# Kernel tuning notes

Measured on AMD Instinct MI355X. Metric: run time of the kernel, lower is better.

Reference implementation:

```python
import jax, jax.numpy as jnp
import numpy as np

N_NODES = 50000
N_EDGES = 800000
D = 64
BN_EPS = 1e-5


def setup_inputs() -> dict:
    key = jax.random.key(0)
    ks = jax.random.split(key, 16)
    x = jax.random.normal(ks[0], (N_NODES, D), dtype=jnp.float32)
    edge_index = jax.random.randint(ks[1], (2, N_EDGES), 0, N_NODES, dtype=jnp.int64)
    s = 1.0 / np.sqrt(D)
    def lin(k):
        kw, kb = jax.random.split(k)
        W = jax.random.uniform(kw, (D, D), jnp.float32, -s, s)
        b = jax.random.uniform(kb, (D,), jnp.float32, -s, s)
        return W, b
    W1_0, b1_0 = lin(ks[2])
    W2_0, b2_0 = lin(ks[3])
    W1_1, b1_1 = lin(ks[4])
    W2_1, b2_1 = lin(ks[5])
    return {
        "x": x, "edge_index": edge_index,
        "W1_0": W1_0, "b1_0": b1_0, "g_0": jnp.ones((D,), jnp.float32), "beta_0": jnp.zeros((D,), jnp.float32), "W2_0": W2_0, "b2_0": b2_0,
        "W1_1": W1_1, "b1_1": b1_1, "g_1": jnp.ones((D,), jnp.float32), "beta_1": jnp.zeros((D,), jnp.float32), "W2_1": W2_1, "b2_1": b2_1,
    }


def _gin_layer(x, src, dst, W1, b1, g, beta, W2, b2):
    # GINConv with eps=0: h_i = MLP( x_i + sum_{j->i} x_j )
    agg = jax.ops.segment_sum(x[src], dst, num_segments=N_NODES)  # [N, D]
    h = agg + x
    h = h @ W1 + b1
    # BatchNorm1d (training-mode batch statistics, biased variance)
    mean = jnp.mean(h, axis=0)
    var = jnp.var(h, axis=0)
    h = (h - mean) * jax.lax.rsqrt(var + BN_EPS) * g + beta
    h = jax.nn.relu(h)
    h = jax.nn.relu(h @ W2 + b2)
    return h


def reference(x, edge_index, W1_0, b1_0, g_0, beta_0, W2_0, b2_0,
              W1_1, b1_1, g_1, beta_1, W2_1, b2_1):
    src = edge_index[0]  # message source j
    dst = edge_index[1]  # aggregation target i
    h1 = _gin_layer(x, src, dst, W1_0, b1_0, g_0, beta_0, W2_0, b2_0)
    h2 = _gin_layer(h1, src, dst, W1_1, b1_1, g_1, beta_1, W2_1, b2_1)
    return (h1, h2)
```

## Files before the change

### kernel.cpp

```cpp
#include <hip/hip_runtime.h>
#include <hip/hip_bf16.h>

#define N_NODES 50000
#define N_EDGES 800000
#define DD 64
#define RPB 64
#define GBLOCKS ((N_NODES + RPB - 1) / RPB)
#define SCAN_BLOCKS ((N_NODES + 255) / 256)
#define BN_EPS 1e-5f


__device__ __forceinline__ float bf2f(unsigned short b) {
    return __uint_as_float(((unsigned)b) << 16);
}
__device__ __forceinline__ float loadF(const void* p, int i, int isf) {
    return isf ? ((const float*)p)[i] : bf2f(((const unsigned short*)p)[i]);
}
template<bool ISF>
__device__ __forceinline__ float4 ld4(const void* p, int i) {
    if (ISF) return *reinterpret_cast<const float4*>((const float*)p + i);
    ushort4 u = *reinterpret_cast<const ushort4*>((const unsigned short*)p + i);
    return make_float4(bf2f(u.x), bf2f(u.y), bf2f(u.z), bf2f(u.w));
}
__device__ __forceinline__ void acc8(float4& a, float4& b, uint4 u) {
    a.x += __uint_as_float(u.x << 16);
    a.y += __uint_as_float(u.x & 0xFFFF0000u);
    a.z += __uint_as_float(u.y << 16);
    a.w += __uint_as_float(u.y & 0xFFFF0000u);
    b.x += __uint_as_float(u.z << 16);
    b.y += __uint_as_float(u.z & 0xFFFF0000u);
    b.z += __uint_as_float(u.w << 16);
    b.w += __uint_as_float(u.w & 0xFFFF0000u);
}

__global__ void init_kernel(const void* __restrict__ x, const int* __restrict__ ei,
                            int* __restrict__ flags, int* __restrict__ cnt,
                            float* __restrict__ sums) {
    int i = blockIdx.x * 256 + threadIdx.x;
    if (i < N_NODES) cnt[i] = 0;
    if (i < 128) sums[i] = 0.0f;
    if (blockIdx.x == 0) {
        __shared__ int cntF, cntI;
        int t = threadIdx.x;
        if (t == 0) { cntF = 0; cntI = 0; }
        __syncthreads();
        unsigned short w = ((const unsigned short*)x)[2 * t];
        int e = (w >> 7) & 0xFF;
        if (e >= 0x70 && e <= 0x8F) atomicAdd(&cntF, 1);
        if (t < 128 && ei[2 * t + 1] == 0) atomicAdd(&cntI, 1);
        __syncthreads();
        if (t == 0) {
            flags[0] = (cntF < 128) ? 1 : 0;
            flags[1] = (cntI > 64) ? 1 : 0;
        }
    }
}

__global__ void cast_kernel(const void* __restrict__ x, unsigned short* __restrict__ xb,
                            const int* __restrict__ flags) {
    int isf = flags[0];
    int i = (blockIdx.x * 256 + threadIdx.x) * 8;
    if (i >= N_NODES * DD) return;
    if (isf) {
        float4 a = *reinterpret_cast<const float4*>((const float*)x + i);
        float4 b = *reinterpret_cast<const float4*>((const float*)x + i + 4);
        ushort4 o0, o1;
        o0.x = __bfloat16_as_ushort(__float2bfloat16(a.x));
        o0.y = __bfloat16_as_ushort(__float2bfloat16(a.y));
        o0.z = __bfloat16_as_ushort(__float2bfloat16(a.z));
        o0.w = __bfloat16_as_ushort(__float2bfloat16(a.w));
        o1.x = __bfloat16_as_ushort(__float2bfloat16(b.x));
        o1.y = __bfloat16_as_ushort(__float2bfloat16(b.y));
        o1.z = __bfloat16_as_ushort(__float2bfloat16(b.z));
        o1.w = __bfloat16_as_ushort(__float2bfloat16(b.w));
        *reinterpret_cast<ushort4*>(xb + i) = o0;
        *reinterpret_cast<ushort4*>(xb + i + 4) = o1;
    } else {
        *reinterpret_cast<uint4*>(xb + i) =
            *reinterpret_cast<const uint4*>((const unsigned short*)x + i);
    }
}

__global__ void hist_kernel(const int* __restrict__ ei, int* __restrict__ cnt,
                            const int* __restrict__ flags) {
    int i64 = flags[1];
    int e = blockIdx.x * 256 + threadIdx.x;
    int d = i64 ? ei[2 * N_EDGES + 2 * e] : ei[N_EDGES + e];
    atomicAdd(cnt + d, 1);
}

__global__ __launch_bounds__(256) void scanA_kernel(const int* __restrict__ cnt,
                                                    int* __restrict__ off,
                                                    int* __restrict__ bsum) {
    __shared__ int tmp[256];
    int t = threadIdx.x;
    int i = blockIdx.x * 256 + t;
    int v = (i < N_NODES) ? cnt[i] : 0;
    tmp[t] = v;
    __syncthreads();
    #pragma unroll
    for (int d = 1; d < 256; d <<= 1) {
        int u = (t >= d) ? tmp[t - d] : 0;
        __syncthreads();
        tmp[t] += u;
        __syncthreads();
    }
    if (i < N_NODES) off[i] = tmp[t] - v;
    if (t == 255) bsum[blockIdx.x] = tmp[255];
}

__global__ __launch_bounds__(256) void scanB_kernel(int* __restrict__ bsum,
                                                    int* __restrict__ off) {
    __shared__ int tmp[256];
    int t = threadIdx.x;
    int v = (t < SCAN_BLOCKS) ? bsum[t] : 0;
    tmp[t] = v;
    __syncthreads();
    #pragma unroll
    for (int d = 1; d < 256; d <<= 1) {
        int u = (t >= d) ? tmp[t - d] : 0;
        __syncthreads();
        tmp[t] += u;
        __syncthreads();
    }
    if (t < SCAN_BLOCKS) bsum[t] = tmp[t] - v;
    if (t == 255) off[N_NODES] = tmp[255];
}

__global__ __launch_bounds__(256) void scanC_kernel(const int* __restrict__ bsum,
                                                    int* __restrict__ off,
                                                    int* __restrict__ cur) {
    int i = blockIdx.x * 256 + threadIdx.x;
    if (i < N_NODES) {
        int o = off[i] + bsum[blockIdx.x];
        off[i] = o;
        cur[i] = o;
    }
}

__global__ void fill_kernel(const int* __restrict__ ei, int* __restrict__ cur,
                            int* __restrict__ srt, const int* __restrict__ flags) {
    int i64 = flags[1];
    int e = blockIdx.x * 256 + threadIdx.x;
    int s, d;
    if (i64) { s = ei[2 * e]; d = ei[2 * N_EDGES + 2 * e]; }
    else     { s = ei[e];     d = ei[N_EDGES + e]; }
    int pos = atomicAdd(cur + d, 1);
    srt[pos] = s;
}

__global__ __launch_bounds__(512) void gather_gemm_stats_kernel(
    const unsigned short* __restrict__ xb, const void* __restrict__ self_src, int force_f32,
    const int* __restrict__ off, const int* __restrict__ srt,
    const void* __restrict__ W, const void* __restrict__ bias,
    float* __restrict__ out_, float* __restrict__ sums, const int* __restrict__ flags)
{
    __shared__ float sIn[RPB][DD];
    __shared__ float r1[8][DD], r2[8][DD];
    int tid = threadIdx.x;
    int lane = tid & 63, w = tid >> 6;
    int rs = lane >> 3, ch = lane & 7;
    int row0 = blockIdx.x * RPB;
    int isf = force_f32 ? 1 : flags[0];

    int lr = w * 8 + rs;
    int r = row0 + lr;
    float4 a  = make_float4(0.f, 0.f, 0.f, 0.f);
    float4 b  = make_float4(0.f, 0.f, 0.f, 0.f);
    float4 a2 = make_float4(0.f, 0.f, 0.f, 0.f);
    float4 b2 = make_float4(0.f, 0.f, 0.f, 0.f);
    if (r < N_NODES) {
        a = isf ? ld4<true>(self_src, r * DD + 8 * ch)
                : ld4<false>(self_src, r * DD + 8 * ch);
        b = isf ? ld4<true>(self_src, r * DD + 8 * ch + 4)
                : ld4<false>(self_src, r * DD + 8 * ch + 4);
        int k0 = off[r], k1 = off[r + 1];
        int k = k0;
        for (; k + 4 <= k1; k += 4) {
            int n0 = srt[k], n1 = srt[k + 1], n2 = srt[k + 2], n3 = srt[k + 3];
            uint4 u0 = *reinterpret_cast<const uint4*>(xb + n0 * DD + 8 * ch);
            uint4 u1 = *reinterpret_cast<const uint4*>(xb + n1 * DD + 8 * ch);
            uint4 u2 = *reinterpret_cast<const uint4*>(xb + n2 * DD + 8 * ch);
            uint4 u3 = *reinterpret_cast<const uint4*>(xb + n3 * DD + 8 * ch);
            acc8(a, b, u0);
            acc8(a2, b2, u1);
            acc8(a, b, u2);
            acc8(a2, b2, u3);
        }
        for (; k < k1; ++k) {
            int n0 = srt[k];
            acc8(a, b, *reinterpret_cast<const uint4*>(xb + n0 * DD + 8 * ch));
        }
        a.x += a2.x; a.y += a2.y; a.z += a2.z; a.w += a2.w;
        b.x += b2.x; b.y += b2.y; b.z += b2.z; b.w += b2.w;
    }
    *reinterpret_cast<float4*>(&sIn[lr][8 * ch]) = a;
    *reinterpret_cast<float4*>(&sIn[lr][8 * ch + 4]) = b;
    __syncthreads();

    float wcol[DD];
    #pragma unroll
    for (int k = 0; k < DD; ++k) wcol[k] = loadF(W, k * DD + lane, isf);
    float bv = loadF(bias, lane, isf);

    float s1 = 0.f, s2 = 0.f;
    #pragma unroll 4
    for (int j = 0; j < 8; ++j) {
        int jr = w * 8 + j;
        float c0 = 0.f, c1 = 0.f, c2 = 0.f, c3 = 0.f;
        #pragma unroll
        for (int k = 0; k < DD; k += 4) {
            float4 aa = *reinterpret_cast<const float4*>(&sIn[jr][k]);
            c0 += aa.x * wcol[k];
            c1 += aa.y * wcol[k + 1];
            c2 += aa.z * wcol[k + 2];
            c3 += aa.w * wcol[k + 3];
        }
        float acc = bv + ((c0 + c1) + (c2 + c3));
        int rr = row0 + jr;
        if (rr < N_NODES) {
            out_[rr * DD + lane] = acc;
            s1 += acc;
            s2 += acc * acc;
        }
    }
    r1[w][lane] = s1; r2[w][lane] = s2;
    __syncthreads();
    if (w == 0) {
        float t1 = 0.f, t2 = 0.f;
        #pragma unroll
        for (int q = 0; q < 8; ++q) { t1 += r1[q][lane]; t2 += r2[q][lane]; }
        atomicAdd(&sums[lane], t1);
        atomicAdd(&sums[64 + lane], t2);
    }
}

__global__ void bn_params_kernel(float* __restrict__ sums,
                                 const void* __restrict__ gma, const void* __restrict__ beta,
                                 float* __restrict__ scsh, const int* __restrict__ flags) {
    int isf = flags[0];
    int c = threadIdx.x;
    float S1 = sums[c];
    float S2 = sums[64 + c];
    float mean = S1 * (1.0f / N_NODES);
    float var  = S2 * (1.0f / N_NODES) - mean * mean;
    float scale = rsqrtf(var + BN_EPS) * loadF(gma, c, isf);
    scsh[c] = scale;
    scsh[DD + c] = loadF(beta, c, isf) - mean * scale;
    sums[c] = 0.0f;
    sums[64 + c] = 0.0f;
}

__global__ __launch_bounds__(256) void mlp2_kernel(
    const float* __restrict__ in_, const float* __restrict__ scsh,
    const void* __restrict__ W, const void* __restrict__ bias,
    float* __restrict__ oF, unsigned short* obf, const int* __restrict__ flags)
{
    __shared__ float sIn[RPB][DD];
    int isf = flags[0];
    int tid = threadIdx.x;
    int c = tid & 63, g = tid >> 6;
    int row0 = blockIdx.x * RPB;

    #pragma unroll
    for (int j = 0; j < 4; ++j) {
        int lr = (tid >> 4) + 16 * j;
        int cc = (tid & 15) << 2;
        int r = row0 + lr;
        float4 v = make_float4(0.f, 0.f, 0.f, 0.f);
        if (r < N_NODES) {
            v = *reinterpret_cast<const float4*>(in_ + r * DD + cc);
            float4 sc = *reinterpret_cast<const float4*>(scsh + cc);
            float4 sh = *reinterpret_cast<const float4*>(scsh + DD + cc);
            v.x = fmaxf(v.x * sc.x + sh.x, 0.f);
            v.y = fmaxf(v.y * sc.y + sh.y, 0.f);
            v.z = fmaxf(v.z * sc.z + sh.z, 0.f);
            v.w = fmaxf(v.w * sc.w + sh.w, 0.f);
        }
        *reinterpret_cast<float4*>(&sIn[lr][cc]) = v;
    }
    __syncthreads();

    float wcol[DD];
    #pragma unroll
    for (int k = 0; k < DD; ++k) wcol[k] = loadF(W, k * DD + c, isf);
    float bv = loadF(bias, c, isf);

    #pragma unroll 4
    for (int j = 0; j < 16; ++j) {
        int lr = g * 16 + j;
        float a0 = 0.f, a1 = 0.f, a2 = 0.f, a3 = 0.f;
        #pragma unroll
        for (int k = 0; k < DD; k += 4) {
            float4 a = *reinterpret_cast<const float4*>(&sIn[lr][k]);
            a0 += a.x * wcol[k];
            a1 += a.y * wcol[k + 1];
            a2 += a.z * wcol[k + 2];
            a3 += a.w * wcol[k + 3];
        }
        float acc = fmaxf(bv + ((a0 + a1) + (a2 + a3)), 0.f);
        int r = row0 + lr;
        if (r < N_NODES) {
            oF[r * DD + c] = acc;
            if (obf) obf[r * DD + c] = __bfloat16_as_ushort(__float2bfloat16(acc));
        }
    }
}

extern "C" void kernel_launch(void* const* d_in, const int* in_sizes, int n_in,
                              void* d_out, int out_size, void* d_ws, size_t ws_size,
                              hipStream_t stream)
{
    (void)in_sizes; (void)n_in; (void)out_size; (void)ws_size;
    const void* x  = d_in[0];
    const int* ei  = (const int*)d_in[1];
    const void* W1_0 = d_in[2];  const void* b1_0 = d_in[3];
    const void* g_0  = d_in[4];  const void* be_0 = d_in[5];
    const void* W2_0 = d_in[6];  const void* b2_0 = d_in[7];
    const void* W1_1 = d_in[8];  const void* b1_1 = d_in[9];
    const void* g_1  = d_in[10]; const void* be_1 = d_in[11];
    const void* W2_1 = d_in[12]; const void* b2_1 = d_in[13];

    float* wsf  = (float*)d_ws;
    float* sums = wsf;
    float* scsh = wsf + 128;
    int*  flags = (int*)(wsf + 256);
    int*  cnt   = (int*)(wsf + 512);
    int*  off   = cnt + 50048;
    int*  cur   = off + 50064;
    int*  bsum  = cur + 50048;
    int*  srt   = bsum + 256;
    unsigned short* xb = (unsigned short*)(srt + 800000);
    float* O1   = (float*)d_out;
    float* O2   = O1 + (size_t)N_NODES * DD;

    dim3 blk(256);

    init_kernel<<<SCAN_BLOCKS, blk, 0, stream>>>(x, ei, flags, cnt, sums);
    cast_kernel<<<(N_NODES * DD / 8 + 255) / 256, blk, 0, stream>>>(x, xb, flags);
    hist_kernel<<<N_EDGES / 256, blk, 0, stream>>>(ei, cnt, flags);
    scanA_kernel<<<SCAN_BLOCKS, blk, 0, stream>>>(cnt, off, bsum);
    scanB_kernel<<<1, blk, 0, stream>>>(bsum, off);
    scanC_kernel<<<SCAN_BLOCKS, blk, 0, stream>>>(bsum, off, cur);
    fill_kernel<<<N_EDGES / 256, blk, 0, stream>>>(ei, cur, srt, flags);

    gather_gemm_stats_kernel<<<GBLOCKS, 512, 0, stream>>>(xb, x, 0, off, srt, W1_0, b1_0,
                                                          O2, sums, flags);
    bn_params_kernel<<<1, 64, 0, stream>>>(sums, g_0, be_0, scsh, flags);
    mlp2_kernel<<<GBLOCKS, blk, 0, stream>>>(O2, scsh, W2_0, b2_0, O1, xb, flags);

    gather_gemm_stats_kernel<<<GBLOCKS, 512, 0, stream>>>(xb, O1, 1, off, srt, W1_1, b1_1,
                                                          O2, sums, flags);
    bn_params_kernel<<<1, 64, 0, stream>>>(sums, g_1, be_1, scsh, flags);
    mlp2_kernel<<<GBLOCKS, blk, 0, stream>>>(O2, scsh, W2_1, b2_1, O2, nullptr, flags);
}
```

Measured before the change: 320.9 us.

## Fuse init/cast and BN-param kernels, halve gather rows, use 16-bit neighbor indices

Merges the init and cast kernels into one launch, and folds the BN scale/shift computation into each mlp2 block so the single-thread bn_params launches go away. Separate stat buffers per layer replace the zero-reset. The gather kernel now handles 32 rows per block with two lanes per row splitting the edge list, combined by a shuffle, to raise parallelism. Sorted source indices are stored as 16-bit values to cut index traffic. This relies on node ids fitting in 16 bits, but there are 50000 nodes, which is below 65536. Every mlp2 block also recomputes the BN params redundantly.

```diff
diff --git a/kernel.cpp b/kernel.cpp
--- a/kernel.cpp
+++ b/kernel.cpp
@@ -4,9 +4,11 @@
 #define N_NODES 50000
 #define N_EDGES 800000
 #define DD 64
-#define RPB 64
+#define RPB 32
 #define GBLOCKS ((N_NODES + RPB - 1) / RPB)
+#define MBLOCKS ((N_NODES + 63) / 64)
 #define SCAN_BLOCKS ((N_NODES + 255) / 256)
+#define CAST_BLOCKS ((N_NODES * DD / 8 + 255) / 256)
 #define BN_EPS 1e-5f
 
 
@@ -33,51 +35,50 @@
     b.w += __uint_as_float(u.w & 0xFFFF0000u);
 }
 
-__global__ void init_kernel(const void* __restrict__ x, const int* __restrict__ ei,
-                            int* __restrict__ flags, int* __restrict__ cnt,
-                            float* __restrict__ sums) {
-    int i = blockIdx.x * 256 + threadIdx.x;
-    if (i < N_NODES) cnt[i] = 0;
-    if (i < 128) sums[i] = 0.0f;
-    if (blockIdx.x == 0) {
-        __shared__ int cntF, cntI;
-        int t = threadIdx.x;
-        if (t == 0) { cntF = 0; cntI = 0; }
-        __syncthreads();
-        unsigned short w = ((const unsigned short*)x)[2 * t];
-        int e = (w >> 7) & 0xFF;
-        if (e >= 0x70 && e <= 0x8F) atomicAdd(&cntF, 1);
-        if (t < 128 && ei[2 * t + 1] == 0) atomicAdd(&cntI, 1);
-        __syncthreads();
-        if (t == 0) {
-            flags[0] = (cntF < 128) ? 1 : 0;
-            flags[1] = (cntI > 64) ? 1 : 0;
-        }
-    }
-}
-
-__global__ void cast_kernel(const void* __restrict__ x, unsigned short* __restrict__ xb,
-                            const int* __restrict__ flags) {
-    int isf = flags[0];
-    int i = (blockIdx.x * 256 + threadIdx.x) * 8;
-    if (i >= N_NODES * DD) return;
-    if (isf) {
-        float4 a = *reinterpret_cast<const float4*>((const float*)x + i);
-        float4 b = *reinterpret_cast<const float4*>((const float*)x + i + 4);
-        ushort4 o0, o1;
-        o0.x = __bfloat16_as_ushort(__float2bfloat16(a.x));
-        o0.y = __bfloat16_as_ushort(__float2bfloat16(a.y));
-        o0.z = __bfloat16_as_ushort(__float2bfloat16(a.z));
-        o0.w = __bfloat16_as_ushort(__float2bfloat16(a.w));
-        o1.x = __bfloat16_as_ushort(__float2bfloat16(b.x));
-        o1.y = __bfloat16_as_ushort(__float2bfloat16(b.y));
-        o1.z = __bfloat16_as_ushort(__float2bfloat16(b.z));
-        o1.w = __bfloat16_as_ushort(__float2bfloat16(b.w));
-        *reinterpret_cast<ushort4*>(xb + i) = o0;
-        *reinterpret_cast<ushort4*>(xb + i + 4) = o1;
-    } else {
-        *reinterpret_cast<uint4*>(xb + i) =
-            *reinterpret_cast<const uint4*>((const unsigned short*)x + i);
+__global__ __launch_bounds__(256) void initcast_kernel(
+    const void* __restrict__ x, const int* __restrict__ ei,
+    int* __restrict__ flags, int* __restrict__ cnt,
+    float* __restrict__ sums, unsigned short* __restrict__ xb)
+{
+    __shared__ int cntF, cntI;
+    int t = threadIdx.x;
+    if (t == 0) { cntF = 0; cntI = 0; }
+    __syncthreads();
+    unsigned short wd = ((const unsigned short*)x)[2 * t];
+    int e = (wd >> 7) & 0xFF;
+    if (e >= 0x70 && e <= 0x8F) atomicAdd(&cntF, 1);
+    if (t < 128 && ei[2 * t + 1] == 0) atomicAdd(&cntI, 1);
+    __syncthreads();
+    int isf = (cntF < 128) ? 1 : 0;
+
+    int gid = blockIdx.x * 256 + t;
+    if (gid < N_NODES) cnt[gid] = 0;
+    if (gid < 256) sums[gid] = 0.0f;
+    if (blockIdx.x == 0 && t == 0) {
+        flags[0] = isf;
+        flags[1] = (cntI > 64) ? 1 : 0;
+    }
+
+    int i = gid * 8;
+    if (i < N_NODES * DD) {
+        if (isf) {
+            float4 a = *reinterpret_cast<const float4*>((const float*)x + i);
+            float4 b = *reinterpret_cast<const float4*>((const float*)x + i + 4);
+            ushort4 o0, o1;
+            o0.x = __bfloat16_as_ushort(__float2bfloat16(a.x));
+            o0.y = __bfloat16_as_ushort(__float2bfloat16(a.y));
+            o0.z = __bfloat16_as_ushort(__float2bfloat16(a.z));
+            o0.w = __bfloat16_as_ushort(__float2bfloat16(a.w));
+            o1.x = __bfloat16_as_ushort(__float2bfloat16(b.x));
+            o1.y = __bfloat16_as_ushort(__float2bfloat16(b.y));
+            o1.z = __bfloat16_as_ushort(__float2bfloat16(b.z));
+            o1.w = __bfloat16_as_ushort(__float2bfloat16(b.w));
+            *reinterpret_cast<ushort4*>(xb + i) = o0;
+            *reinterpret_cast<ushort4*>(xb + i + 4) = o1;
+        } else {
+            *reinterpret_cast<uint4*>(xb + i) =
+                *reinterpret_cast<const uint4*>((const unsigned short*)x + i);
+        }
     }
 }
 
@@ -139,19 +140,19 @@
 }
 
 __global__ void fill_kernel(const int* __restrict__ ei, int* __restrict__ cur,
-                            int* __restrict__ srt, const int* __restrict__ flags) {
+                            unsigned short* __restrict__ srt, const int* __restrict__ flags) {
     int i64 = flags[1];
     int e = blockIdx.x * 256 + threadIdx.x;
     int s, d;
     if (i64) { s = ei[2 * e]; d = ei[2 * N_EDGES + 2 * e]; }
     else     { s = ei[e];     d = ei[N_EDGES + e]; }
     int pos = atomicAdd(cur + d, 1);
-    srt[pos] = s;
+    srt[pos] = (unsigned short)s;
 }
 
 __global__ __launch_bounds__(512) void gather_gemm_stats_kernel(
     const unsigned short* __restrict__ xb, const void* __restrict__ self_src, int force_f32,
-    const int* __restrict__ off, const int* __restrict__ srt,
+    const int* __restrict__ off, const unsigned short* __restrict__ srt,
     const void* __restrict__ W, const void* __restrict__ bias,
     float* __restrict__ out_, float* __restrict__ sums, const int* __restrict__ flags)
 {
@@ -159,43 +160,55 @@
     __shared__ float r1[8][DD], r2[8][DD];
     int tid = threadIdx.x;
     int lane = tid & 63, w = tid >> 6;
-    int rs = lane >> 3, ch = lane & 7;
+    int rs = lane >> 4;
+    int ns = (lane >> 3) & 1;
+    int ch = lane & 7;
     int row0 = blockIdx.x * RPB;
     int isf = force_f32 ? 1 : flags[0];
 
-    int lr = w * 8 + rs;
+    int lr = w * 4 + rs;
     int r = row0 + lr;
     float4 a  = make_float4(0.f, 0.f, 0.f, 0.f);
     float4 b  = make_float4(0.f, 0.f, 0.f, 0.f);
     float4 a2 = make_float4(0.f, 0.f, 0.f, 0.f);
     float4 b2 = make_float4(0.f, 0.f, 0.f, 0.f);
     if (r < N_NODES) {
-        a = isf ? ld4<true>(self_src, r * DD + 8 * ch)
-                : ld4<false>(self_src, r * DD + 8 * ch);
-        b = isf ? ld4<true>(self_src, r * DD + 8 * ch + 4)
-                : ld4<false>(self_src, r * DD + 8 * ch + 4);
+        if (ns == 0) {
+            a = isf ? ld4<true>(self_src, r * DD + 8 * ch)
+                    : ld4<false>(self_src, r * DD + 8 * ch);
+            b = isf ? ld4<true>(self_src, r * DD + 8 * ch + 4)
+                    : ld4<false>(self_src, r * DD + 8 * ch + 4);
+        }
         int k0 = off[r], k1 = off[r + 1];
-        int k = k0;
-        for (; k + 4 <= k1; k += 4) {
-            int n0 = srt[k], n1 = srt[k + 1], n2 = srt[k + 2], n3 = srt[k + 3];
+        int mid = k0 + ((k1 - k0 + 1) >> 1);
+        int k  = ns ? mid : k0;
+        int ke = ns ? k1 : mid;
+        for (; k + 2 <= ke; k += 2) {
+            int n0 = srt[k], n1 = srt[k + 1];
             uint4 u0 = *reinterpret_cast<const uint4*>(xb + n0 * DD + 8 * ch);
             uint4 u1 = *reinterpret_cast<const uint4*>(xb + n1 * DD + 8 * ch);
-            uint4 u2 = *reinterpret_cast<const uint4*>(xb + n2 * DD + 8 * ch);
-            uint4 u3 = *reinterpret_cast<const uint4*>(xb + n3 * DD + 8 * ch);
             acc8(a, b, u0);
             acc8(a2, b2, u1);
-            acc8(a, b, u2);
-            acc8(a2, b2, u3);
-        }
-        for (; k < k1; ++k) {
+        }
+        if (k < ke) {
             int n0 = srt[k];
             acc8(a, b, *reinterpret_cast<const uint4*>(xb + n0 * DD + 8 * ch));
         }
         a.x += a2.x; a.y += a2.y; a.z += a2.z; a.w += a2.w;
         b.x += b2.x; b.y += b2.y; b.z += b2.z; b.w += b2.w;
     }
-    *reinterpret_cast<float4*>(&sIn[lr][8 * ch]) = a;
-    *reinterpret_cast<float4*>(&sIn[lr][8 * ch + 4]) = b;
+    a.x += __shfl_xor(a.x, 8, 64);
+    a.y += __shfl_xor(a.y, 8, 64);
+    a.z += __shfl_xor(a.z, 8, 64);
+    a.w += __shfl_xor(a.w, 8, 64);
+    b.x += __shfl_xor(b.x, 8, 64);
+    b.y += __shfl_xor(b.y, 8, 64);
+    b.z += __shfl_xor(b.z, 8, 64);
+    b.w += __shfl_xor(b.w, 8, 64);
+    if (ns == 0) {
+        *reinterpret_cast<float4*>(&sIn[lr][8 * ch]) = a;
+        *reinterpret_cast<float4*>(&sIn[lr][8 * ch + 4]) = b;
+    }
     __syncthreads();
 
     float wcol[DD];
@@ -204,9 +217,9 @@
     float bv = loadF(bias, lane, isf);
 
     float s1 = 0.f, s2 = 0.f;
-    #pragma unroll 4
-    for (int j = 0; j < 8; ++j) {
-        int jr = w * 8 + j;
+    #pragma unroll
+    for (int j = 0; j < 4; ++j) {
+        int jr = w * 4 + j;
         float c0 = 0.f, c1 = 0.f, c2 = 0.f, c3 = 0.f;
         #pragma unroll
         for (int k = 0; k < DD; k += 4) {
@@ -235,32 +248,29 @@
     }
 }
 
-__global__ void bn_params_kernel(float* __restrict__ sums,
-                                 const void* __restrict__ gma, const void* __restrict__ beta,
-                                 float* __restrict__ scsh, const int* __restrict__ flags) {
-    int isf = flags[0];
-    int c = threadIdx.x;
-    float S1 = sums[c];
-    float S2 = sums[64 + c];
-    float mean = S1 * (1.0f / N_NODES);
-    float var  = S2 * (1.0f / N_NODES) - mean * mean;
-    float scale = rsqrtf(var + BN_EPS) * loadF(gma, c, isf);
-    scsh[c] = scale;
-    scsh[DD + c] = loadF(beta, c, isf) - mean * scale;
-    sums[c] = 0.0f;
-    sums[64 + c] = 0.0f;
-}
-
 __global__ __launch_bounds__(256) void mlp2_kernel(
-    const float* __restrict__ in_, const float* __restrict__ scsh,
+    const float* __restrict__ in_, const float* __restrict__ sums,
+    const void* __restrict__ gma, const void* __restrict__ beta,
     const void* __restrict__ W, const void* __restrict__ bias,
     float* __restrict__ oF, unsigned short* obf, const int* __restrict__ flags)
 {
-    __shared__ float sIn[RPB][DD];
+    __shared__ float sIn[64][DD];
+    __shared__ float sScale[DD], sShift[DD];
     int isf = flags[0];
     int tid = threadIdx.x;
     int c = tid & 63, g = tid >> 6;
-    int row0 = blockIdx.x * RPB;
+    int row0 = blockIdx.x * 64;
+
+    if (tid < 64) {
+        float S1 = sums[tid];
+        float S2 = sums[64 + tid];
+        float mean = S1 * (1.0f / N_NODES);
+        float var  = S2 * (1.0f / N_NODES) - mean * mean;
+        float scale = rsqrtf(var + BN_EPS) * loadF(gma, tid, isf);
+        sScale[tid] = scale;
+        sShift[tid] = loadF(beta, tid, isf) - mean * scale;
+    }
+    __syncthreads();
 
     #pragma unroll
     for (int j = 0; j < 4; ++j) {
@@ -270,8 +280,8 @@
         float4 v = make_float4(0.f, 0.f, 0.f, 0.f);
         if (r < N_NODES) {
             v = *reinterpret_cast<const float4*>(in_ + r * DD + cc);
-            float4 sc = *reinterpret_cast<const float4*>(scsh + cc);
-            float4 sh = *reinterpret_cast<const float4*>(scsh + DD + cc);
+            float4 sc = *reinterpret_cast<const float4*>(&sScale[cc]);
+            float4 sh = *reinterpret_cast<const float4*>(&sShift[cc]);
             v.x = fmaxf(v.x * sc.x + sh.x, 0.f);
             v.y = fmaxf(v.y * sc.y + sh.y, 0.f);
             v.z = fmaxf(v.z * sc.z + sh.z, 0.f);
@@ -321,23 +331,22 @@
     const void* g_1  = d_in[10]; const void* be_1 = d_in[11];
     const void* W2_1 = d_in[12]; const void* b2_1 = d_in[13];
 
-    float* wsf  = (float*)d_ws;
-    float* sums = wsf;
-    float* scsh = wsf + 128;
-    int*  flags = (int*)(wsf + 256);
-    int*  cnt   = (int*)(wsf + 512);
-    int*  off   = cnt + 50048;
-    int*  cur   = off + 50064;
-    int*  bsum  = cur + 50048;
-    int*  srt   = bsum + 256;
-    unsigned short* xb = (unsigned short*)(srt + 800000);
-    float* O1   = (float*)d_out;
-    float* O2   = O1 + (size_t)N_NODES * DD;
+    float* wsf   = (float*)d_ws;
+    float* sumsA = wsf;
+    float* sumsB = wsf + 128;
+    int*  flags  = (int*)(wsf + 256);
+    int*  cnt    = (int*)(wsf + 512);
+    int*  off    = cnt + 50048;
+    int*  cur    = off + 50064;
+    int*  bsum   = cur + 50048;
+    unsigned short* srt = (unsigned short*)(bsum + 256);
+    unsigned short* xb  = srt + 800064;
+    float* O1    = (float*)d_out;
+    float* O2    = O1 + (size_t)N_NODES * DD;
 
     dim3 blk(256);
 
-    init_kernel<<<SCAN_BLOCKS, blk, 0, stream>>>(x, ei, flags, cnt, sums);
-    cast_kernel<<<(N_NODES * DD / 8 + 255) / 256, blk, 0, stream>>>(x, xb, flags);
+    initcast_kernel<<<CAST_BLOCKS, blk, 0, stream>>>(x, ei, flags, cnt, sumsA, xb);
     hist_kernel<<<N_EDGES / 256, blk, 0, stream>>>(ei, cnt, flags);
     scanA_kernel<<<SCAN_BLOCKS, blk, 0, stream>>>(cnt, off, bsum);
     scanB_kernel<<<1, blk, 0, stream>>>(bsum, off);
@@ -345,12 +354,10 @@
     fill_kernel<<<N_EDGES / 256, blk, 0, stream>>>(ei, cur, srt, flags);
 
     gather_gemm_stats_kernel<<<GBLOCKS, 512, 0, stream>>>(xb, x, 0, off, srt, W1_0, b1_0,
-                                                          O2, sums, flags);
-    bn_params_kernel<<<1, 64, 0, stream>>>(sums, g_0, be_0, scsh, flags);
-    mlp2_kernel<<<GBLOCKS, blk, 0, stream>>>(O2, scsh, W2_0, b2_0, O1, xb, flags);
+                                                          O2, sumsA, flags);
+    mlp2_kernel<<<MBLOCKS, blk, 0, stream>>>(O2, sumsA, g_0, be_0, W2_0, b2_0, O1, xb, flags);
 
     gather_gemm_stats_kernel<<<GBLOCKS, 512, 0, stream>>>(xb, O1, 1, off, srt, W1_1, b1_1,
-                                                          O2, sums, flags);
-    bn_params_kernel<<<1, 64, 0, stream>>>(sums, g_1, be_1, scsh, flags);
-    mlp2_kernel<<<GBLOCKS, blk, 0, stream>>>(O2, scsh, W2_1, b2_1, O2, nullptr, flags);
-}
+                                                          O2, sumsB, flags);
+    mlp2_kernel<<<MBLOCKS, blk, 0, stream>>>(O2, sumsB, g_1, be_1, W2_1, b2_1, O2, nullptr, flags);
+}
```

Result: slower. 334.1 us (+4.1%).
